# Kernel optimization log

Hardware: AMD Instinct MI355X
Metric: run time of the kernel (lower is better)

Reference implementation:

```python
import jax, jax.numpy as jnp
import numpy as np
import math

B, T, E, HS = 8, 2048, 1024, 64  # batch, seq, n_embd, head_size (n_embd // n_head)


def setup_inputs() -> dict:
    key = jax.random.key(0)
    ks = jax.random.split(key, 7)
    sc = 1.0 / math.sqrt(E)  # roughly nn.Linear init scale
    return {
        "inputs": jax.random.normal(ks[0], (B, T, E), dtype=jnp.float32),
        "Wq": jax.random.normal(ks[1], (HS, E), dtype=jnp.float32) * sc,
        "bq": jax.random.normal(ks[2], (HS,), dtype=jnp.float32) * sc,
        "Wk": jax.random.normal(ks[3], (HS, E), dtype=jnp.float32) * sc,
        "bk": jax.random.normal(ks[4], (HS,), dtype=jnp.float32) * sc,
        "Wv": jax.random.normal(ks[5], (HS, E), dtype=jnp.float32) * sc,
        "bv": jax.random.normal(ks[6], (HS,), dtype=jnp.float32) * sc,
    }


def reference(inputs, Wq, bq, Wk, bk, Wv, bv):
    # Linear projections: x @ W.T + b  -> [B, T, HS]
    q = jnp.einsum("bte,he->bth", inputs, Wq) + bq
    k = jnp.einsum("bte,he->bth", inputs, Wk) + bk
    v = jnp.einsum("bte,he->bth", inputs, Wv) + bv

    # Scaled scores: [B, T, T]
    scores = jnp.einsum("bqh,bkh->bqk", q, k) / math.sqrt(HS)

    # Causal mask exactly as original: scores * tril - 1e12 * (1 - tril)
    tril = jnp.tril(jnp.ones((T, T), dtype=scores.dtype))
    scores = scores * tril - 1e12 * (1.0 - tril)

    attn = jax.nn.softmax(scores, axis=-1)
    # dropout p=0 (eval) -> identity
    out = jnp.einsum("bqk,bkh->bqh", attn, v)  # [B, T, HS]
    return out
```

## Files before the change

kernel.cpp:

```cpp
#include <hip/hip_runtime.h>
#include <hip/hip_bf16.h>


typedef __attribute__((ext_vector_type(8))) short short8;
typedef __attribute__((ext_vector_type(4))) float f32x4;

#if __has_builtin(__builtin_amdgcn_exp2f)
#define EXP2(x) __builtin_amdgcn_exp2f(x)
#else
#define EXP2(x) exp2f(x)
#endif

#define QSCALE 0.18033688f

__device__ inline unsigned short f2bf(float f) {
    unsigned int u = __builtin_bit_cast(unsigned int, f);
    u += 0x7FFF + ((u >> 16) & 1);
    return (unsigned short)(u >> 16);
}

__global__ __launch_bounds__(64) void prep_w(
    const float* __restrict__ Wq, const float* __restrict__ Wk,
    const float* __restrict__ Wv, unsigned short* __restrict__ Wfrag)
{
    const int ct = blockIdx.x >> 5;
    const int kk = blockIdx.x & 31;
    const int L  = threadIdx.x;
    const int l16 = L & 15, quad = L >> 4;
    const int col = ct * 16 + l16;

    const float* W; int row; float scale = 1.0f;
    if (col < 64)       { W = Wq; row = col;       scale = QSCALE; }
    else if (col < 128) { W = Wk; row = col - 64; }
    else                { W = Wv; row = col - 128; }

    const float* p = W + (size_t)row * 1024 + kk * 32 + quad * 8;
    alignas(16) unsigned short tmp[8];
    #pragma unroll
    for (int j = 0; j < 8; j++) tmp[j] = f2bf(p[j] * scale);
    unsigned short* dst = Wfrag + ((size_t)blockIdx.x * 64 + L) * 8;
    *reinterpret_cast<int4*>(dst) = *reinterpret_cast<const int4*>(tmp);
}

#define XLD 1032
__global__ __launch_bounds__(256, 4) void qkv_kernel(
    const float* __restrict__ x, const unsigned short* __restrict__ Wfrag,
    const float* __restrict__ bq, const float* __restrict__ bk,
    const float* __restrict__ bv,
    unsigned short* __restrict__ Qb, unsigned short* __restrict__ Kb,
    unsigned short* __restrict__ Vt)
{
    __shared__ alignas(16) unsigned short xs[32][XLD];

    const int tid  = threadIdx.x;
    const int m0   = blockIdx.x * 32;
    const int lane = tid & 63;
    const int w    = tid >> 6;
    const int l16  = lane & 15, quad = lane >> 4;

    #pragma unroll
    for (int i = 0; i < 16; i++) {
        int ch  = tid + 256 * i;
        int r   = ch >> 7;
        int c16 = ch & 127;
        const float* p = x + (size_t)(m0 + r) * 1024 + c16 * 8;
        float4 v0 = *reinterpret_cast<const float4*>(p);
        float4 v1 = *reinterpret_cast<const float4*>(p + 4);
        alignas(16) unsigned short t8[8] = {
            f2bf(v0.x), f2bf(v0.y), f2bf(v0.z), f2bf(v0.w),
            f2bf(v1.x), f2bf(v1.y), f2bf(v1.z), f2bf(v1.w)};
        *reinterpret_cast<int4*>(&xs[r][c16 * 8]) =
            *reinterpret_cast<const int4*>(t8);
    }
    __syncthreads();

    const int ct0 = w * 3;
    f32x4 acc[2][3];
    #pragma unroll
    for (int a = 0; a < 2; a++)
        #pragma unroll
        for (int c = 0; c < 3; c++) acc[a][c] = (f32x4){0.f, 0.f, 0.f, 0.f};

    short8 bcur[3];
    #pragma unroll
    for (int ci = 0; ci < 3; ci++)
        bcur[ci] = *reinterpret_cast<const short8*>(
            Wfrag + ((size_t)((ct0 + ci) * 32) * 64 + lane) * 8);

    for (int kk = 0; kk < 32; kk++) {
        const int kkn = (kk < 31) ? kk + 1 : 31;
        short8 bnxt[3];
        #pragma unroll
        for (int ci = 0; ci < 3; ci++)
            bnxt[ci] = *reinterpret_cast<const short8*>(
                Wfrag + ((size_t)((ct0 + ci) * 32 + kkn) * 64 + lane) * 8);

        short8 a0 = *reinterpret_cast<const short8*>(&xs[l16][kk * 32 + quad * 8]);
        short8 a1 = *reinterpret_cast<const short8*>(&xs[16 + l16][kk * 32 + quad * 8]);
        #pragma unroll
        for (int ci = 0; ci < 3; ci++) {
            acc[0][ci] = __builtin_amdgcn_mfma_f32_16x16x32_bf16(a0, bcur[ci], acc[0][ci], 0, 0, 0);
            acc[1][ci] = __builtin_amdgcn_mfma_f32_16x16x32_bf16(a1, bcur[ci], acc[1][ci], 0, 0, 0);
        }
        #pragma unroll
        for (int ci = 0; ci < 3; ci++) bcur[ci] = bnxt[ci];
    }

    const int bi = m0 >> 11;
    const int t0 = m0 & 2047;
    #pragma unroll
    for (int rt = 0; rt < 2; rt++) {
        #pragma unroll
        for (int ci = 0; ci < 3; ci++) {
            const int ct = ct0 + ci;
            const int h  = (ct & 3) * 16 + l16;
            if (ct < 4) {
                float bias = bq[h] * QSCALE;
                #pragma unroll
                for (int i = 0; i < 4; i++) {
                    size_t m = (size_t)(m0 + rt * 16 + quad * 4 + i);
                    Qb[m * 64 + h] = f2bf(acc[rt][ci][i] + bias);
                }
            } else if (ct < 8) {
                float bias = bk[h];
                #pragma unroll
                for (int i = 0; i < 4; i++) {
                    size_t m = (size_t)(m0 + rt * 16 + quad * 4 + i);
                    Kb[m * 64 + h] = f2bf(acc[rt][ci][i] + bias);
                }
            } else {
                float bias = bv[h];
                alignas(8) unsigned short tmp[4];
                #pragma unroll
                for (int i = 0; i < 4; i++) tmp[i] = f2bf(acc[rt][ci][i] + bias);
                unsigned short* dst = Vt + ((size_t)(bi * 64 + h)) * 2048
                                     + t0 + rt * 16 + quad * 4;
                *reinterpret_cast<int2*>(dst) = *reinterpret_cast<const int2*>(tmp);
            }
        }
    }
}

__global__ __launch_bounds__(64, 3) void attn_part(
    const unsigned short* __restrict__ Qb,
    const unsigned short* __restrict__ Kb,
    const unsigned short* __restrict__ Vt,
    float* __restrict__ Opart, float* __restrict__ Lpart)
{
    __shared__ alignas(16) unsigned short ps[16][72];

    const int bid = blockIdx.x;
    const int b   = bid & 7;
    const int j16 = (bid >> 3) & 127;
    const int c   = bid >> 10;
    const int nkt = (j16 >> 2) + 1;
    const int kt0 = c * 8;
    if (kt0 >= nkt) return;
    const int kt1 = (kt0 + 8 < nkt) ? kt0 + 8 : nkt;

    const int q0  = j16 * 16;
    const int L   = threadIdx.x;
    const int l16 = L & 15, quad = L >> 4;

    const unsigned short* qrow = Qb + ((size_t)(b * 2048 + q0 + l16)) * 64 + quad * 8;
    short8 aq0 = *reinterpret_cast<const short8*>(qrow);
    short8 aq1 = *reinterpret_cast<const short8*>(qrow + 32);

    const unsigned short* Kbat = Kb + (size_t)b * 2048 * 64;
    const unsigned short* Vbat = Vt + (size_t)b * 64 * 2048;

    f32x4 o[4];
    float rs[4] = {0.f, 0.f, 0.f, 0.f};
    #pragma unroll
    for (int i = 0; i < 4; i++) o[i] = (f32x4){0, 0, 0, 0};

    short8 kf[8];
    {
        const unsigned short* kfr = Kbat + ((size_t)(kt0 * 64 + l16)) * 64 + quad * 8;
        #pragma unroll
        for (int ks2 = 0; ks2 < 2; ks2++)
            #pragma unroll
            for (int ct = 0; ct < 4; ct++)
                kf[ks2 * 4 + ct] = *reinterpret_cast<const short8*>(
                    kfr + (size_t)(ct * 16) * 64 + ks2 * 32);
    }

    for (int kt = kt0; kt < kt1; kt++) {
        const int ktn = (kt + 1 < kt1) ? kt + 1 : kt;
        const unsigned short* kfrn = Kbat + ((size_t)(ktn * 64 + l16)) * 64 + quad * 8;
        short8 kn[8];
        #pragma unroll
        for (int ks2 = 0; ks2 < 2; ks2++)
            #pragma unroll
            for (int ct = 0; ct < 4; ct++)
                kn[ks2 * 4 + ct] = *reinterpret_cast<const short8*>(
                    kfrn + (size_t)(ct * 16) * 64 + ks2 * 32);

        const unsigned short* vfr = Vbat + (size_t)l16 * 2048 + kt * 64 + quad * 8;
        short8 vf[8];
        #pragma unroll
        for (int ks2 = 0; ks2 < 2; ks2++)
            #pragma unroll
            for (int ct = 0; ct < 4; ct++)
                vf[ks2 * 4 + ct] = *reinterpret_cast<const short8*>(
                    vfr + (size_t)(ct * 16) * 2048 + ks2 * 32);

        f32x4 s[4];
        #pragma unroll
        for (int ct = 0; ct < 4; ct++) s[ct] = (f32x4){0, 0, 0, 0};
        #pragma unroll
        for (int ks2 = 0; ks2 < 2; ks2++) {
            short8 aqf = ks2 ? aq1 : aq0;
            #pragma unroll
            for (int ct = 0; ct < 4; ct++)
                s[ct] = __builtin_amdgcn_mfma_f32_16x16x32_bf16(
                    aqf, kf[ks2 * 4 + ct], s[ct], 0, 0, 0);
        }

        if (kt == nkt - 1) {
            #pragma unroll
            for (int ct = 0; ct < 4; ct++) {
                int col = kt * 64 + ct * 16 + l16;
                #pragma unroll
                for (int i = 0; i < 4; i++) {
                    int row = q0 + quad * 4 + i;
                    if (col > row) s[ct][i] = -1e30f;
                }
            }
        }

        #pragma unroll
        for (int ct = 0; ct < 4; ct++) {
            #pragma unroll
            for (int i = 0; i < 4; i++) {
                float p = EXP2(s[ct][i]);
                rs[i] += p;
                ps[quad * 4 + i][ct * 16 + l16] = f2bf(p);
            }
        }

        short8 ap0 = *reinterpret_cast<const short8*>(&ps[l16][quad * 8]);
        short8 ap1 = *reinterpret_cast<const short8*>(&ps[l16][32 + quad * 8]);

        #pragma unroll
        for (int ks2 = 0; ks2 < 2; ks2++) {
            short8 apf = ks2 ? ap1 : ap0;
            #pragma unroll
            for (int ct = 0; ct < 4; ct++)
                o[ct] = __builtin_amdgcn_mfma_f32_16x16x32_bf16(
                    apf, vf[ks2 * 4 + ct], o[ct], 0, 0, 0);
        }

        #pragma unroll
        for (int j = 0; j < 8; j++) kf[j] = kn[j];
    }

    float* op = Opart + (size_t)bid * 1024;
    #pragma unroll
    for (int i = 0; i < 4; i++) {
        int r = quad * 4 + i;
        #pragma unroll
        for (int ct = 0; ct < 4; ct++)
            op[(size_t)r * 64 + ct * 16 + l16] = o[ct][i];
        float v = rs[i];
        v += __shfl_xor(v, 1);
        v += __shfl_xor(v, 2);
        v += __shfl_xor(v, 4);
        v += __shfl_xor(v, 8);
        if (l16 == 0) Lpart[(size_t)bid * 16 + r] = v;
    }
}

__global__ __launch_bounds__(256) void attn_combine(
    const float* __restrict__ Opart, const float* __restrict__ Lpart,
    float* __restrict__ out)
{
    const int t0 = blockIdx.x * 256 + threadIdx.x;
    #pragma unroll
    for (int it = 0; it < 2; it++) {
        const int v    = t0 + it * 131072;
        const int flat = v * 4;
        const int b    = flat >> 17;
        const int rem  = flat & 131071;
        const int t    = rem >> 6;
        const int h0   = rem & 63;
        const int j16  = t >> 4, row = t & 15;
        const int nch  = ((j16 >> 2) + 8) >> 3;
        const int pidb = (j16 << 3) | b;

        float4 acc = {0.f, 0.f, 0.f, 0.f};
        float  l   = 0.f;
        for (int c = 0; c < nch; c++) {
            const int pid = (c << 10) | pidb;
            const float* op = Opart + (size_t)pid * 1024 + row * 64 + h0;
            float4 x4 = *reinterpret_cast<const float4*>(op);
            acc.x += x4.x; acc.y += x4.y; acc.z += x4.z; acc.w += x4.w;
            l += Lpart[(size_t)pid * 16 + row];
        }
        const float inv = 1.f / l;
        float4 r = {acc.x * inv, acc.y * inv, acc.z * inv, acc.w * inv};
        *reinterpret_cast<float4*>(out + flat) = r;
    }
}

extern "C" void kernel_launch(void* const* d_in, const int* in_sizes, int n_in,
                              void* d_out, int out_size, void* d_ws, size_t ws_size,
                              hipStream_t stream) {
    const float* x  = (const float*)d_in[0];
    const float* Wq = (const float*)d_in[1];
    const float* bq = (const float*)d_in[2];
    const float* Wk = (const float*)d_in[3];
    const float* bk = (const float*)d_in[4];
    const float* Wv = (const float*)d_in[5];
    const float* bv = (const float*)d_in[6];
    float* out = (float*)d_out;

    unsigned short* Qb    = (unsigned short*)d_ws;
    unsigned short* Kb    = Qb + (size_t)16384 * 64;
    unsigned short* Vt    = Kb + (size_t)16384 * 64;
    unsigned short* Wfrag = Vt + (size_t)16384 * 64;
    float* Opart = (float*)(Wfrag + (size_t)12 * 32 * 64 * 8);
    float* Lpart = Opart + (size_t)4096 * 1024;

    prep_w<<<384, 64, 0, stream>>>(Wq, Wk, Wv, Wfrag);
    qkv_kernel<<<512, 256, 0, stream>>>(x, Wfrag, bq, bk, bv, Qb, Kb, Vt);
    attn_part<<<4096, 64, 0, stream>>>(Qb, Kb, Vt, Opart, Lpart);
    attn_combine<<<512, 256, 0, stream>>>(Opart, Lpart, out);
}
```

Measured before the change: 159.2 us.

## Store K/V in MFMA fragment layout and group four query tiles per block

The QKV kernel now writes K and V directly in a pre-swizzled per-64-key-tile fragment layout, so each lane in the attention kernel loads its operand with one contiguous 16-byte read per fragment instead of strided row or column reads. The attention kernel moves from 64-thread blocks covering one 16-row query tile to 256-thread blocks whose four waves cover four adjacent query tiles that share the same key range, which improves L2/cache locality for K/V and cuts block count. This adds scattered 2-byte stores in the QKV epilogue for K and couples the causal work of the four waves, which can cause some imbalance within a block.

```diff
diff --git a/kernel.cpp b/kernel.cpp
--- a/kernel.cpp
+++ b/kernel.cpp
@@ -47,8 +47,8 @@
     const float* __restrict__ x, const unsigned short* __restrict__ Wfrag,
     const float* __restrict__ bq, const float* __restrict__ bk,
     const float* __restrict__ bv,
-    unsigned short* __restrict__ Qb, unsigned short* __restrict__ Kb,
-    unsigned short* __restrict__ Vt)
+    unsigned short* __restrict__ Qb, unsigned short* __restrict__ Kf,
+    unsigned short* __restrict__ Vf)
 {
     __shared__ alignas(16) unsigned short xs[32][XLD];
 
@@ -107,7 +107,6 @@
     }
 
     const int bi = m0 >> 11;
-    const int t0 = m0 & 2047;
     #pragma unroll
     for (int rt = 0; rt < 2; rt++) {
         #pragma unroll
@@ -125,85 +124,92 @@
                 float bias = bk[h];
                 #pragma unroll
                 for (int i = 0; i < 4; i++) {
-                    size_t m = (size_t)(m0 + rt * 16 + quad * 4 + i);
-                    Kb[m * 64 + h] = f2bf(acc[rt][ci][i] + bias);
+                    int t   = m0 + rt * 16 + quad * 4 + i;
+                    int tin = t & 63;
+                    int kt  = (t & 2047) >> 6;
+                    int f   = ((h >> 5) << 2) | (tin >> 4);
+                    int lp  = (tin & 15) | (((h >> 3) & 3) << 4);
+                    Kf[(((size_t)(bi * 32 + kt) * 8 + f) * 64 + lp) * 8 + (h & 7)]
+                        = f2bf(acc[rt][ci][i] + bias);
                 }
             } else {
                 float bias = bv[h];
+                int tb  = m0 + rt * 16 + quad * 4;
+                int tin = tb & 63;
+                int kt  = (tb & 2047) >> 6;
+                int f   = ((tin >> 5) << 2) | (h >> 4);
+                int lp  = (h & 15) | (((tin >> 3) & 3) << 4);
                 alignas(8) unsigned short tmp[4];
                 #pragma unroll
                 for (int i = 0; i < 4; i++) tmp[i] = f2bf(acc[rt][ci][i] + bias);
-                unsigned short* dst = Vt + ((size_t)(bi * 64 + h)) * 2048
-                                     + t0 + rt * 16 + quad * 4;
+                unsigned short* dst =
+                    Vf + (((size_t)(bi * 32 + kt) * 8 + f) * 64 + lp) * 8 + (tin & 7);
                 *reinterpret_cast<int2*>(dst) = *reinterpret_cast<const int2*>(tmp);
             }
         }
     }
 }
 
-__global__ __launch_bounds__(64, 3) void attn_part(
+__global__ __launch_bounds__(256, 3) void attn_part(
     const unsigned short* __restrict__ Qb,
-    const unsigned short* __restrict__ Kb,
-    const unsigned short* __restrict__ Vt,
+    const unsigned short* __restrict__ Kf,
+    const unsigned short* __restrict__ Vf,
     float* __restrict__ Opart, float* __restrict__ Lpart)
 {
-    __shared__ alignas(16) unsigned short ps[16][72];
+    __shared__ alignas(16) unsigned short ps[4][16][72];
 
     const int bid = blockIdx.x;
     const int b   = bid & 7;
-    const int j16 = (bid >> 3) & 127;
-    const int c   = bid >> 10;
-    const int nkt = (j16 >> 2) + 1;
+    const int j64 = (bid >> 3) & 31;
+    const int c   = bid >> 8;
+    const int nkt = j64 + 1;
     const int kt0 = c * 8;
     if (kt0 >= nkt) return;
     const int kt1 = (kt0 + 8 < nkt) ? kt0 + 8 : nkt;
 
-    const int q0  = j16 * 16;
-    const int L   = threadIdx.x;
-    const int l16 = L & 15, quad = L >> 4;
+    const int tid  = threadIdx.x;
+    const int w    = tid >> 6;
+    const int lane = tid & 63;
+    const int l16  = lane & 15, quad = lane >> 4;
+    const int j16  = j64 * 4 + w;
+    const int q0   = j16 * 16;
 
     const unsigned short* qrow = Qb + ((size_t)(b * 2048 + q0 + l16)) * 64 + quad * 8;
     short8 aq0 = *reinterpret_cast<const short8*>(qrow);
     short8 aq1 = *reinterpret_cast<const short8*>(qrow + 32);
 
-    const unsigned short* Kbat = Kb + (size_t)b * 2048 * 64;
-    const unsigned short* Vbat = Vt + (size_t)b * 64 * 2048;
+    const unsigned short* Kbat = Kf + (size_t)(b * 32) * 4096;
+    const unsigned short* Vbat = Vf + (size_t)(b * 32) * 4096;
 
     f32x4 o[4];
     float rs[4] = {0.f, 0.f, 0.f, 0.f};
     #pragma unroll
     for (int i = 0; i < 4; i++) o[i] = (f32x4){0, 0, 0, 0};
 
-    short8 kf[8];
+    short8 kfr[8];
     {
-        const unsigned short* kfr = Kbat + ((size_t)(kt0 * 64 + l16)) * 64 + quad * 8;
-        #pragma unroll
-        for (int ks2 = 0; ks2 < 2; ks2++)
-            #pragma unroll
-            for (int ct = 0; ct < 4; ct++)
-                kf[ks2 * 4 + ct] = *reinterpret_cast<const short8*>(
-                    kfr + (size_t)(ct * 16) * 64 + ks2 * 32);
+        const unsigned short* kb = Kbat + (size_t)kt0 * 4096 + lane * 8;
+        #pragma unroll
+        for (int f = 0; f < 8; f++)
+            kfr[f] = *reinterpret_cast<const short8*>(kb + f * 512);
     }
 
     for (int kt = kt0; kt < kt1; kt++) {
         const int ktn = (kt + 1 < kt1) ? kt + 1 : kt;
-        const unsigned short* kfrn = Kbat + ((size_t)(ktn * 64 + l16)) * 64 + quad * 8;
         short8 kn[8];
-        #pragma unroll
-        for (int ks2 = 0; ks2 < 2; ks2++)
-            #pragma unroll
-            for (int ct = 0; ct < 4; ct++)
-                kn[ks2 * 4 + ct] = *reinterpret_cast<const short8*>(
-                    kfrn + (size_t)(ct * 16) * 64 + ks2 * 32);
-
-        const unsigned short* vfr = Vbat + (size_t)l16 * 2048 + kt * 64 + quad * 8;
-        short8 vf[8];
-        #pragma unroll
-        for (int ks2 = 0; ks2 < 2; ks2++)
-            #pragma unroll
-            for (int ct = 0; ct < 4; ct++)
-                vf[ks2 * 4 + ct] = *reinterpret_cast<const short8*>(
-                    vfr + (size_t)(ct * 16) * 2048 + ks2 * 32);
+        {
+            const unsigned short* kb = Kbat + (size_t)ktn * 4096 + lane * 8;
+            #pragma unroll
+            for (int f = 0; f < 8; f++)
+                kn[f] = *reinterpret_cast<const short8*>(kb + f * 512);
+        }
+        short8 vfr[8];
+        {
+            const unsigned short* vb = Vbat + (size_t)kt * 4096 + lane * 8;
+            #pragma unroll
+            for (int f = 0; f < 8; f++)
+                vfr[f] = *reinterpret_cast<const short8*>(vb + f * 512);
+        }
 
         f32x4 s[4];
         #pragma unroll
@@ -214,7 +220,7 @@
             #pragma unroll
             for (int ct = 0; ct < 4; ct++)
                 s[ct] = __builtin_amdgcn_mfma_f32_16x16x32_bf16(
-                    aqf, kf[ks2 * 4 + ct], s[ct], 0, 0, 0);
+                    aqf, kfr[ks2 * 4 + ct], s[ct], 0, 0, 0);
         }
 
         if (kt == nkt - 1) {
@@ -235,12 +241,12 @@
             for (int i = 0; i < 4; i++) {
                 float p = EXP2(s[ct][i]);
                 rs[i] += p;
-                ps[quad * 4 + i][ct * 16 + l16] = f2bf(p);
+                ps[w][quad * 4 + i][ct * 16 + l16] = f2bf(p);
             }
         }
 
-        short8 ap0 = *reinterpret_cast<const short8*>(&ps[l16][quad * 8]);
-        short8 ap1 = *reinterpret_cast<const short8*>(&ps[l16][32 + quad * 8]);
+        short8 ap0 = *reinterpret_cast<const short8*>(&ps[w][l16][quad * 8]);
+        short8 ap1 = *reinterpret_cast<const short8*>(&ps[w][l16][32 + quad * 8]);
 
         #pragma unroll
         for (int ks2 = 0; ks2 < 2; ks2++) {
@@ -248,14 +254,15 @@
             #pragma unroll
             for (int ct = 0; ct < 4; ct++)
                 o[ct] = __builtin_amdgcn_mfma_f32_16x16x32_bf16(
-                    apf, vf[ks2 * 4 + ct], o[ct], 0, 0, 0);
-        }
-
-        #pragma unroll
-        for (int j = 0; j < 8; j++) kf[j] = kn[j];
-    }
-
-    float* op = Opart + (size_t)bid * 1024;
+                    apf, vfr[ks2 * 4 + ct], o[ct], 0, 0, 0);
+        }
+
+        #pragma unroll
+        for (int f = 0; f < 8; f++) kfr[f] = kn[f];
+    }
+
+    const int pid = (c << 10) | (j16 << 3) | b;
+    float* op = Opart + (size_t)pid * 1024;
     #pragma unroll
     for (int i = 0; i < 4; i++) {
         int r = quad * 4 + i;
@@ -267,7 +274,7 @@
         v += __shfl_xor(v, 2);
         v += __shfl_xor(v, 4);
         v += __shfl_xor(v, 8);
-        if (l16 == 0) Lpart[(size_t)bid * 16 + r] = v;
+        if (l16 == 0) Lpart[(size_t)pid * 16 + r] = v;
     }
 }
 
@@ -316,14 +323,14 @@
     float* out = (float*)d_out;
 
     unsigned short* Qb    = (unsigned short*)d_ws;
-    unsigned short* Kb    = Qb + (size_t)16384 * 64;
-    unsigned short* Vt    = Kb + (size_t)16384 * 64;
-    unsigned short* Wfrag = Vt + (size_t)16384 * 64;
+    unsigned short* Kf    = Qb + (size_t)16384 * 64;
+    unsigned short* Vf    = Kf + (size_t)16384 * 64;
+    unsigned short* Wfrag = Vf + (size_t)16384 * 64;
     float* Opart = (float*)(Wfrag + (size_t)12 * 32 * 64 * 8);
     float* Lpart = Opart + (size_t)4096 * 1024;
 
     prep_w<<<384, 64, 0, stream>>>(Wq, Wk, Wv, Wfrag);
-    qkv_kernel<<<512, 256, 0, stream>>>(x, Wfrag, bq, bk, bv, Qb, Kb, Vt);
-    attn_part<<<4096, 64, 0, stream>>>(Qb, Kb, Vt, Opart, Lpart);
+    qkv_kernel<<<512, 256, 0, stream>>>(x, Wfrag, bq, bk, bv, Qb, Kf, Vf);
+    attn_part<<<1024, 256, 0, stream>>>(Qb, Kf, Vf, Opart, Lpart);
     attn_combine<<<512, 256, 0, stream>>>(Opart, Lpart, out);
 }
```

Result: faster. 138.7 us (-12.8%).
